# Kernel tuning notes

Measured on AMD Instinct MI355X. Metric: run time of the kernel, lower is better.

## Reference

```python
import jax, jax.numpy as jnp
import numpy as np

B, L, D, H, NL, FUT, MD = 4096, 64, 16, 128, 2, 30, 2
HEAD_IN = D + H  # 144


def setup_inputs() -> dict:
    key = jax.random.key(0)
    ks = jax.random.split(key, 20)
    g = lambda k, *sh: jax.random.normal(k, sh, dtype=jnp.float32) * 0.05
    return {
        'history': jax.random.normal(ks[0], (B, L, D), dtype=jnp.float32),
        'history_mask': jnp.ones((B, L), dtype=jnp.float32),
        'Wp': g(ks[1], D, H), 'bp': jnp.zeros((H,), jnp.float32),
        # stacked gate weights: order [f, i, o, c]
        'Wx': g(ks[2], NL, 4, H, H), 'bx': jnp.zeros((NL, 4, H), jnp.float32),
        'Uh': g(ks[3], NL, 4, H, H),
        'Wd': g(ks[4], NL, H, H), 'bd': jnp.zeros((NL, H), jnp.float32),
        'Wt': g(ks[5], NL, H), 'bt': jnp.zeros((NL, H), jnp.float32),
        'ln_g': jnp.ones((HEAD_IN,), jnp.float32), 'ln_b': jnp.zeros((HEAD_IN,), jnp.float32),
        'W1': g(ks[6], HEAD_IN, H), 'b1': jnp.zeros((H,), jnp.float32),
        'W2': g(ks[7], H, FUT * MD), 'b2': jnp.zeros((FUT * MD,), jnp.float32),
    }


def _forward(history, history_mask, Wp, bp, Wx, bx, Uh, Wd, bd, Wt, bt,
             ln_g, ln_b, W1, b1, W2, b2):
    x = history @ Wp + bp                                 # [B,L,H]
    delta = jnp.clip(history[..., 5], 0.0)[..., None]     # [B,L,1]
    mask = history_mask[..., None]                        # [B,L,1]
    e = jnp.float32(np.e)

    def step(carry, inp):
        h, c = carry                                      # each [NL,B,H]
        xt, dt, mt = inp                                  # [B,H],[B,1],[B,1]
        decay = 1.0 / jnp.log(e + dt)                     # [B,1]
        step_in = xt
        hs, cs = [], []
        for l in range(NL):
            z = (jnp.einsum('bh,ghk->gbk', step_in, Wx[l]) + bx[l][:, None, :]
                 + jnp.einsum('bh,ghk->gbk', h[l], Uh[l]))  # [4,B,H]
            f_t = jax.nn.sigmoid(z[0])
            i_t = jax.nn.sigmoid(z[1])
            o_t = jax.nn.sigmoid(z[2])
            c_tilde = jnp.tanh(z[3])
            h_tilde = c_tilde + i_t
            h_short = jnp.tanh(h_tilde @ Wd[l] + bd[l])
            d_t = jax.nn.sigmoid(decay * Wt[l] + bt[l])   # [B,H]
            h_star = (h_tilde - h_short) + h_short * d_t
            c_new = jnp.tanh(h_star + o_t * c[l])
            h_new = o_t * jnp.tanh(c_new)
            h_l = mt * h_new + (1.0 - mt) * h[l]
            c_l = mt * c_new + (1.0 - mt) * c[l]
            hs.append(h_l)
            cs.append(c_l)
            step_in = h_l
        return (jnp.stack(hs), jnp.stack(cs)), step_in

    h0 = jnp.zeros((NL, B, H), x.dtype)
    c0 = jnp.zeros((NL, B, H), x.dtype)
    xs = (x.transpose(1, 0, 2), delta.transpose(1, 0, 2), mask.transpose(1, 0, 2))
    _, outs = jax.lax.scan(step, (h0, c0), xs)            # [L,B,H]
    encoded = outs.transpose(1, 0, 2) * mask              # [B,L,H]

    # decoder state: last valid obs + hidden
    counts = jnp.clip(history_mask.sum(axis=1), 1, L).astype(jnp.int32)
    last = counts - 1
    bi = jnp.arange(B)
    state = jnp.concatenate([history[bi, last, :], encoded[bi, last, :]], axis=-1)

    # forecast head: LayerNorm -> Linear -> ReLU -> Linear
    mu = state.mean(axis=-1, keepdims=True)
    var = state.var(axis=-1, keepdims=True)
    sn = (state - mu) * jax.lax.rsqrt(var + 1e-5) * ln_g + ln_b
    pred = jax.nn.relu(sn @ W1 + b1) @ W2 + b2
    pred = pred.reshape(B, FUT, MD)
    return jnp.nan_to_num(pred, nan=0.0, posinf=1e4, neginf=-1e4)


def reference(history, history_mask, Wp, bp, Wx, bx, Uh, Wd, bd, Wt, bt,
              ln_g, ln_b, W1, b1, W2, b2):
    return _forward(history, history_mask, Wp, bp, Wx, bx, Uh, Wd, bd, Wt, bt,
                    ln_g, ln_b, W1, b1, W2, b2)
```

## Files before the change

### kernel.cpp

```cpp
#include <hip/hip_runtime.h>
#include <hip/hip_bf16.h>


typedef __bf16 bf16x8 __attribute__((ext_vector_type(8)));
typedef float  f32x4  __attribute__((ext_vector_type(4)));

__device__ __forceinline__ f32x4 mfma16(bf16x8 a, bf16x8 b, f32x4 c) {
  return __builtin_amdgcn_mfma_f32_16x16x32_bf16(a, b, c, 0, 0, 0);
}

#if __has_builtin(__builtin_amdgcn_exp2f)
__device__ __forceinline__ float fexp2(float x) { return __builtin_amdgcn_exp2f(x); }
#else
__device__ __forceinline__ float fexp2(float x) { return exp2f(x); }
#endif
#if __has_builtin(__builtin_amdgcn_rcpf)
__device__ __forceinline__ float frcp(float x) { return __builtin_amdgcn_rcpf(x); }
#else
__device__ __forceinline__ float frcp(float x) { return __fdividef(1.f, x); }
#endif
__device__ __forceinline__ float sigmE(float u) { return frcp(1.f + fexp2(u)); }
__device__ __forceinline__ float tanhE(float u) {
  return __fmaf_rn(-2.f, frcp(1.f + fexp2(u)), 1.f);
}
#define SCL_S (-1.44269504f)
#define SCL_T (2.88539008f)

#define OFF_BWD0 122880
#define OFF_BT1  155648
#define OFF_BWD1 352256
#define OFF_BZ0  385024

#define S_WB0   0
#define S_AH    122880
#define S_A0H   125440
#define S_A1H   129792
#define S_AT0   134144
#define S_AT1   138496
#define S_DM    142848
#define S_LAST  143232
#define S_TOTAL 143296
#define S_STATE 0
#define S_A1L   9216
#define S_REDS  17408
#define S_REDQ  18432

__device__ __forceinline__ int bt0f_off(int n, int k) {
  int g = n >> 7, w = (n >> 4) & 7, c = n & 15;
  int kk = k >> 5, q = (k >> 3) & 3, j = k & 7;
  return ((w * 3 + g) * 5 + kk) * 512 + (q * 16 + c) * 8 + j;
}

__global__ void tlstm_prep(const float* __restrict__ Wp, const float* __restrict__ bp,
                           const float* __restrict__ Wx, const float* __restrict__ bx,
                           const float* __restrict__ Uh, const float* __restrict__ Wd,
                           __bf16* __restrict__ BT0f, __bf16* __restrict__ BWd0,
                           __bf16* __restrict__ BT1, __bf16* __restrict__ BWd1,
                           float* __restrict__ bz0) {
  if (blockIdx.x < 26) {
    int idx = blockIdx.x * 256 + threadIdx.x;
    if (idx >= 384 * 17) return;
    int kk = idx / 384, n = idx - kk * 384;
    int npr = n & 127, g = n >> 7, gs = g + 1;
    float sg = (g == 2) ? SCL_T : SCL_S;
    const float* wxg = Wx + (gs * 128) * 128 + npr;
    if (kk < 16) {
      const float* wprow = Wp + kk * 128;
      float s = 0.f;
      for (int h = 0; h < 128; ++h) s += wprow[h] * wxg[h * 128];
      BT0f[bt0f_off(n, kk)] = (__bf16)(s * sg);
    } else {
      float s = bx[gs * 128 + npr];
      for (int h = 0; h < 128; ++h) s += bp[h] * wxg[h * 128];
      bz0[n] = s * sg;
      for (int k2 = 16; k2 < 32; ++k2) BT0f[bt0f_off(n, k2)] = (__bf16)0.f;
    }
    return;
  }
  int e = (blockIdx.x - 26) * 256 + threadIdx.x;
  if (e < 49152) {
    int k = e / 384, n = e - k * 384;
    int npr = n & 127, g = n >> 7, gs = g + 1;
    float sg = (g == 2) ? SCL_T : SCL_S;
    BT0f[bt0f_off(n, k + 32)] = (__bf16)(Uh[(gs * 128 + k) * 128 + npr] * sg);
  } else if (e < 65536) {
    int e2 = e - 49152; int k = e2 >> 7, n = e2 & 127;
    BWd0[n * 128 + k] = (__bf16)(Wd[k * 128 + n] * SCL_T);
  } else if (e < 163840) {
    int e2 = e - 65536; int k = e2 / 384, n = e2 - k * 384;
    int npr = n & 127, g = n >> 7, gs = g + 1;
    float sg = (g == 2) ? SCL_T : SCL_S;
    float v = (k < 128) ? Wx[((4 + gs) * 128 + k) * 128 + npr]
                        : Uh[((4 + gs) * 128 + (k - 128)) * 128 + npr];
    BT1[n * 256 + k] = (__bf16)(v * sg);
  } else if (e < 180224) {
    int e2 = e - 163840; int k = e2 >> 7, n = e2 & 127;
    BWd1[n * 128 + k] = (__bf16)(Wd[(128 + k) * 128 + n] * SCL_T);
  }
}

__global__ __launch_bounds__(512, 1) void tlstm_main(
    const float* __restrict__ hist, const float* __restrict__ hmask,
    const __bf16* __restrict__ BT0f, const __bf16* __restrict__ BWd0,
    const __bf16* __restrict__ BT1, const __bf16* __restrict__ BWd1,
    const float* __restrict__ bz0, const float* __restrict__ bx,
    const float* __restrict__ bd, const float* __restrict__ Wt,
    const float* __restrict__ bt, const float* __restrict__ lng,
    const float* __restrict__ lnb, const float* __restrict__ W1,
    const float* __restrict__ b1, const float* __restrict__ W2,
    const float* __restrict__ b2, float* __restrict__ out) {
  extern __shared__ __align__(16) char smem[];
  __bf16* WB0 = (__bf16*)(smem + S_WB0);
  __bf16 (*AH)[16][40]  = (__bf16(*)[16][40])(smem + S_AH);
  __bf16 (*A0H)[136]    = (__bf16(*)[136])(smem + S_A0H);
  __bf16 (*A1H)[136]    = (__bf16(*)[136])(smem + S_A1H);
  __bf16 (*AT0)[136]    = (__bf16(*)[136])(smem + S_AT0);
  __bf16 (*AT1)[136]    = (__bf16(*)[136])(smem + S_AT1);
  float (*dmL)[2][16]   = (float(*)[2][16])(smem + S_DM);
  int*   lastL          = (int*)(smem + S_LAST);
  float (*stateL)[144]  = (float(*)[144])(smem + S_STATE);
  float (*a1L)[128]     = (float(*)[128])(smem + S_A1L);
  float (*redS)[16]     = (float(*)[16])(smem + S_REDS);
  float (*redQ)[16]     = (float(*)[16])(smem + S_REDQ);

  const int tid  = threadIdx.x;
  const int wave = tid >> 6;
  const int lane = tid & 63;
  const int q    = lane >> 4;
  const int c16  = lane & 15;
  const int q8   = q * 8;
  const int b0   = blockIdx.x * 16;
  const int nc   = wave * 16 + c16;

  for (int i = tid * 8; i < 61440; i += 4096)
    *(bf16x8*)(WB0 + i) = *(const bf16x8*)(BT0f + i);
  {
    __bf16* z = (__bf16*)(smem + S_AH);
    for (int i = tid; i < 5632; i += 512) z[i] = (__bf16)0.f;
  }
  if (tid < 16) {
    float s = 0.f;
    for (int t = 0; t < 64; ++t) s += hmask[(b0 + tid) * 64 + t];
    s = fminf(fmaxf(s, 1.f), 64.f);
    lastL[tid] = (int)s - 1;
  }

  float bz0r[3], bz1r[3];
#pragma unroll
  for (int g = 0; g < 3; ++g) {
    float sg = (g == 2) ? SCL_T : SCL_S;
    bz0r[g] = bz0[g * 128 + nc];
    bz1r[g] = bx[(5 + g) * 128 + nc] * sg;
  }
  const float bd0r = bd[nc] * SCL_T,       bd1r = bd[128 + nc] * SCL_T;
  const float wt0r = Wt[nc] * SCL_S,       wt1r = Wt[128 + nc] * SCL_S;
  const float bt0r = bt[nc] * SCL_S,       bt1r = bt[128 + nc] * SCL_S;

  int offW[3];
#pragma unroll
  for (int g = 0; g < 3; ++g) offW[g] = ((wave * 3 + g) * 5) * 512 + lane * 8;

  bf16x8 wf1[24], bwd0[4], bwd1[4];
#pragma unroll
  for (int g = 0; g < 3; ++g)
#pragma unroll
    for (int kk = 0; kk < 8; ++kk)
      wf1[g * 8 + kk] = *(const bf16x8*)(BT1 + (g * 128 + nc) * 256 + kk * 32 + q8);
#pragma unroll
  for (int kk = 0; kk < 4; ++kk) {
    bwd0[kk] = *(const bf16x8*)(BWd0 + nc * 128 + q8 + kk * 32);
    bwd1[kk] = *(const bf16x8*)(BWd1 + nc * 128 + q8 + kk * 32);
  }

  float h0r[4] = {}, c0r[4] = {}, h1r[4] = {}, c1r[4] = {}, encr[4] = {};

  __syncthreads();

  int lrow[4];
#pragma unroll
  for (int r = 0; r < 4; ++r) lrow[r] = lastL[q * 4 + r];

  const int srow = (tid >> 4) & 15, scol = tid & 15;
  const float* histrow = hist + (long)(b0 + srow) * 1024 + scol;
  const float* hmrow   = hmask + (long)(b0 + srow) * 64;

  float hv = 0.f, mv = 0.f;
  if (tid < 256) {
    float v0 = histrow[0];
    AH[0][srow][scol] = (__bf16)v0;
    if (scol == 5)
      dmL[0][0][srow] = __fdividef(1.f, __logf(2.7182818284590452f + fmaxf(v0, 0.f)));
    if (scol == 0) dmL[0][1][srow] = hmrow[0];
    hv = histrow[16];
    mv = hmrow[1];
  }
  __syncthreads();

  for (int t = 0; t <= 64; ++t) {
    const int p = t & 1, pn = p ^ 1;
    const int sp = t % 3, sm = (t + 2) % 3, sn = (t + 1) % 3;

    float otl0[4], otl1[4];
    if (t > 0) {
      f32x4 acc[3];
#pragma unroll
      for (int g = 0; g < 3; ++g) acc[g] = (f32x4){bz1r[g], bz1r[g], bz1r[g], bz1r[g]};
#pragma unroll
      for (int kk = 0; kk < 4; ++kk) {
        bf16x8 a = *(const bf16x8*)&A0H[c16][kk * 32 + q8];
#pragma unroll
        for (int g = 0; g < 3; ++g) acc[g] = mfma16(a, wf1[g * 8 + kk], acc[g]);
      }
#pragma unroll
      for (int kk = 0; kk < 4; ++kk) {
        bf16x8 a = *(const bf16x8*)&A1H[c16][kk * 32 + q8];
#pragma unroll
        for (int g = 0; g < 3; ++g) acc[g] = mfma16(a, wf1[g * 8 + 4 + kk], acc[g]);
      }
#pragma unroll
      for (int r = 0; r < 4; ++r) {
        float ht = tanhE(acc[2][r]) + sigmE(acc[0][r]);
        otl1[r] = sigmE(acc[1][r]);
        AT1[q * 4 + r][nc] = (__bf16)ht;
      }
    }
    if (t < 64) {
      f32x4 acc[3];
#pragma unroll
      for (int g = 0; g < 3; ++g) acc[g] = (f32x4){bz0r[g], bz0r[g], bz0r[g], bz0r[g]};
      {
        bf16x8 a = *(const bf16x8*)&AH[p][c16][q8];
#pragma unroll
        for (int g = 0; g < 3; ++g)
          acc[g] = mfma16(a, *(const bf16x8*)(WB0 + offW[g]), acc[g]);
      }
#pragma unroll
      for (int kk = 0; kk < 4; ++kk) {
        bf16x8 a = *(const bf16x8*)&A0H[c16][kk * 32 + q8];
#pragma unroll
        for (int g = 0; g < 3; ++g)
          acc[g] = mfma16(a, *(const bf16x8*)(WB0 + offW[g] + (kk + 1) * 512), acc[g]);
      }
#pragma unroll
      for (int r = 0; r < 4; ++r) {
        float ht = tanhE(acc[2][r]) + sigmE(acc[0][r]);
        otl0[r] = sigmE(acc[1][r]);
        AT0[q * 4 + r][nc] = (__bf16)ht;
      }
    }
    __syncthreads();

    if (t < 64) {
      float drow[4], mrow[4];
#pragma unroll
      for (int r = 0; r < 4; ++r) {
        drow[r] = dmL[sp][0][q * 4 + r];
        mrow[r] = dmL[sp][1][q * 4 + r];
      }
      f32x4 accd = (f32x4){bd0r, bd0r, bd0r, bd0r};
#pragma unroll
      for (int kk = 0; kk < 4; ++kk) {
        bf16x8 a = *(const bf16x8*)&AT0[c16][kk * 32 + q8];
        accd = mfma16(a, bwd0[kk], accd);
      }
#pragma unroll
      for (int r = 0; r < 4; ++r) {
        float htl   = (float)AT0[q * 4 + r][nc];
        float hs    = tanhE(accd[r]);
        float dgate = sigmE(__fmaf_rn(drow[r], wt0r, bt0r));
        float hstar = __fmaf_rn(hs, dgate - 1.f, htl);
        float cn    = tanhE(SCL_T * __fmaf_rn(otl0[r], c0r[r], hstar));
        float hn    = otl0[r] * tanhE(SCL_T * cn);
        float m     = mrow[r];
        float hl    = __fmaf_rn(m, hn - h0r[r], h0r[r]);
        float cl    = __fmaf_rn(m, cn - c0r[r], c0r[r]);
        h0r[r] = hl; c0r[r] = cl;
        A0H[q * 4 + r][nc] = (__bf16)hl;
      }
    }
    if (t > 0) {
      float dpre[4], mpre[4];
#pragma unroll
      for (int r = 0; r < 4; ++r) {
        dpre[r] = dmL[sm][0][q * 4 + r];
        mpre[r] = dmL[sm][1][q * 4 + r];
      }
      f32x4 accd = (f32x4){bd1r, bd1r, bd1r, bd1r};
#pragma unroll
      for (int kk = 0; kk < 4; ++kk) {
        bf16x8 a = *(const bf16x8*)&AT1[c16][kk * 32 + q8];
        accd = mfma16(a, bwd1[kk], accd);
      }
      const int tm1 = t - 1;
#pragma unroll
      for (int r = 0; r < 4; ++r) {
        float htl   = (float)AT1[q * 4 + r][nc];
        float hs    = tanhE(accd[r]);
        float dgate = sigmE(__fmaf_rn(dpre[r], wt1r, bt1r));
        float hstar = __fmaf_rn(hs, dgate - 1.f, htl);
        float cn    = tanhE(SCL_T * __fmaf_rn(otl1[r], c1r[r], hstar));
        float hn    = otl1[r] * tanhE(SCL_T * cn);
        float m     = mpre[r];
        float hl    = __fmaf_rn(m, hn - h1r[r], h1r[r]);
        float cl    = __fmaf_rn(m, cn - c1r[r], c1r[r]);
        h1r[r] = hl; c1r[r] = cl;
        A1H[q * 4 + r][nc] = (__bf16)hl;
        if (tm1 == lrow[r]) encr[r] = hl * m;
      }
    }
    if (tid < 256 && t < 63) {
      AH[pn][srow][scol] = (__bf16)hv;
      if (scol == 5)
        dmL[sn][0][srow] = __fdividef(1.f, __logf(2.7182818284590452f + fmaxf(hv, 0.f)));
      if (scol == 0) dmL[sn][1][srow] = mv;
      if (t < 62) { hv = histrow[(t + 2) * 16]; mv = hmrow[t + 2]; }
    }
    __syncthreads();
  }

  if (tid < 256)
    stateL[srow][scol] = hist[((long)(b0 + srow) * 64 + lastL[srow]) * 16 + scol];
#pragma unroll
  for (int r = 0; r < 4; ++r)
    stateL[q * 4 + r][16 + nc] = encr[r];
  __syncthreads();

  if (tid < 256) {
    float sm2 = 0.f, sq = 0.f;
    for (int k = scol; k < 144; k += 16) {
      float v = stateL[srow][k];
      sm2 += v; sq += v * v;
    }
    redS[srow][scol] = sm2; redQ[srow][scol] = sq;
  }
  __syncthreads();
  if (tid < 16) {
    float sm2 = 0.f, sq = 0.f;
    for (int s2 = 0; s2 < 16; ++s2) { sm2 += redS[tid][s2]; sq += redQ[tid][s2]; }
    float mu  = sm2 * (1.f / 144.f);
    float var = sq * (1.f / 144.f) - mu * mu;
    redS[0][tid] = mu;
    redQ[0][tid] = rsqrtf(var + 1e-5f);
  }
  __syncthreads();
  if (tid < 256) {
    float mu = redS[0][srow], rs = redQ[0][srow];
    for (int k = scol; k < 144; k += 16)
      stateL[srow][k] = (stateL[srow][k] - mu) * rs * lng[k] + lnb[k];
  }
  __syncthreads();
  if (tid < 256) {
    float accw[8];
#pragma unroll
    for (int o = 0; o < 8; ++o) accw[o] = b1[scol + 16 * o];
    for (int k = 0; k < 144; ++k) {
      float sv = stateL[srow][k];
      const float* w = W1 + k * 128 + scol;
#pragma unroll
      for (int o = 0; o < 8; ++o) accw[o] += sv * w[16 * o];
    }
#pragma unroll
    for (int o = 0; o < 8; ++o) a1L[srow][scol + 16 * o] = fmaxf(accw[o], 0.f);
  }
  __syncthreads();
  for (int e = tid; e < 960; e += 512) {
    int row = e / 60, j = e - row * 60;
    float accv = b2[j];
    for (int k = 0; k < 128; ++k) accv += a1L[row][k] * W2[k * 60 + j];
    accv = (accv != accv) ? 0.f : fminf(fmaxf(accv, -1e4f), 1e4f);
    out[(b0 + row) * 60 + j] = accv;
  }
}

extern "C" void kernel_launch(void* const* d_in, const int* in_sizes, int n_in,
                              void* d_out, int out_size, void* d_ws, size_t ws_size,
                              hipStream_t stream) {
  const float* hist  = (const float*)d_in[0];
  const float* hmask = (const float*)d_in[1];
  const float* Wp    = (const float*)d_in[2];
  const float* bp    = (const float*)d_in[3];
  const float* Wx    = (const float*)d_in[4];
  const float* bx    = (const float*)d_in[5];
  const float* Uh    = (const float*)d_in[6];
  const float* Wd    = (const float*)d_in[7];
  const float* bd    = (const float*)d_in[8];
  const float* Wt    = (const float*)d_in[9];
  const float* bt    = (const float*)d_in[10];
  const float* lng   = (const float*)d_in[11];
  const float* lnb   = (const float*)d_in[12];
  const float* W1    = (const float*)d_in[13];
  const float* b1    = (const float*)d_in[14];
  const float* W2    = (const float*)d_in[15];
  const float* b2    = (const float*)d_in[16];
  float* out = (float*)d_out;

  char* ws = (char*)d_ws;
  __bf16* BT0f = (__bf16*)ws;
  __bf16* BWd0 = (__bf16*)(ws + OFF_BWD0);
  __bf16* BT1  = (__bf16*)(ws + OFF_BT1);
  __bf16* BWd1 = (__bf16*)(ws + OFF_BWD1);
  float*  bz0  = (float*)(ws + OFF_BZ0);

  hipFuncSetAttribute((const void*)tlstm_main,
                      hipFuncAttributeMaxDynamicSharedMemorySize, S_TOTAL);

  tlstm_prep<<<730, 256, 0, stream>>>(Wp, bp, Wx, bx, Uh, Wd,
                                      BT0f, BWd0, BT1, BWd1, bz0);
  tlstm_main<<<256, 512, S_TOTAL, stream>>>(hist, hmask, BT0f, BWd0, BT1, BWd1,
                                            bz0, bx, bd, Wt, bt, lng, lnb,
                                            W1, b1, W2, b2, out);
}
```

Baseline: 300.1 us.

## Split the two LSTM layers across separate wave groups in a 1024-thread block

Doubles the block to 1024 threads and gives layer 0 to waves 0-7 and layer 1 to waves 8-15, so each wave runs one layer's MFMA and elementwise work per step instead of both. Each thread now keeps only one layer's weights and state in registers, which relieves register pressure, and the two layers' work runs on different waves inside the same barrier-delimited phases. The cost is twice as many waves to synchronise at each barrier and a register budget capped by the 1024-thread launch bound, which may cause spills in the layer-1 group that holds 24 weight fragments.

```diff
diff --git a/kernel.cpp b/kernel.cpp
--- a/kernel.cpp
+++ b/kernel.cpp
@@ -99,7 +99,7 @@
   }
 }
 
-__global__ __launch_bounds__(512, 1) void tlstm_main(
+__global__ __launch_bounds__(1024, 1) void tlstm_main(
     const float* __restrict__ hist, const float* __restrict__ hmask,
     const __bf16* __restrict__ BT0f, const __bf16* __restrict__ BWd0,
     const __bf16* __restrict__ BT1, const __bf16* __restrict__ BWd1,
@@ -124,19 +124,20 @@
   float (*redQ)[16]     = (float(*)[16])(smem + S_REDQ);
 
   const int tid  = threadIdx.x;
-  const int wave = tid >> 6;
+  const int grp  = tid >> 9;
+  const int w8   = (tid >> 6) & 7;
   const int lane = tid & 63;
   const int q    = lane >> 4;
   const int c16  = lane & 15;
   const int q8   = q * 8;
   const int b0   = blockIdx.x * 16;
-  const int nc   = wave * 16 + c16;
-
-  for (int i = tid * 8; i < 61440; i += 4096)
+  const int nc   = w8 * 16 + c16;
+
+  for (int i = tid * 8; i < 61440; i += 8192)
     *(bf16x8*)(WB0 + i) = *(const bf16x8*)(BT0f + i);
   {
     __bf16* z = (__bf16*)(smem + S_AH);
-    for (int i = tid; i < 5632; i += 512) z[i] = (__bf16)0.f;
+    for (int i = tid; i < 5632; i += 1024) z[i] = (__bf16)0.f;
   }
   if (tid < 16) {
     float s = 0.f;
@@ -145,34 +146,42 @@
     lastL[tid] = (int)s - 1;
   }
 
-  float bz0r[3], bz1r[3];
-#pragma unroll
-  for (int g = 0; g < 3; ++g) {
-    float sg = (g == 2) ? SCL_T : SCL_S;
-    bz0r[g] = bz0[g * 128 + nc];
-    bz1r[g] = bx[(5 + g) * 128 + nc] * sg;
-  }
-  const float bd0r = bd[nc] * SCL_T,       bd1r = bd[128 + nc] * SCL_T;
-  const float wt0r = Wt[nc] * SCL_S,       wt1r = Wt[128 + nc] * SCL_S;
-  const float bt0r = bt[nc] * SCL_S,       bt1r = bt[128 + nc] * SCL_S;
+  const int lo = grp * 128;
+  float bzr[3];
+  if (grp == 0) {
+#pragma unroll
+    for (int g = 0; g < 3; ++g) bzr[g] = bz0[g * 128 + nc];
+  } else {
+#pragma unroll
+    for (int g = 0; g < 3; ++g) {
+      float sg = (g == 2) ? SCL_T : SCL_S;
+      bzr[g] = bx[(5 + g) * 128 + nc] * sg;
+    }
+  }
+  const float bdr = bd[lo + nc] * SCL_T;
+  const float wtr = Wt[lo + nc] * SCL_S;
+  const float btr = bt[lo + nc] * SCL_S;
 
   int offW[3];
-#pragma unroll
-  for (int g = 0; g < 3; ++g) offW[g] = ((wave * 3 + g) * 5) * 512 + lane * 8;
-
-  bf16x8 wf1[24], bwd0[4], bwd1[4];
-#pragma unroll
-  for (int g = 0; g < 3; ++g)
-#pragma unroll
-    for (int kk = 0; kk < 8; ++kk)
-      wf1[g * 8 + kk] = *(const bf16x8*)(BT1 + (g * 128 + nc) * 256 + kk * 32 + q8);
-#pragma unroll
-  for (int kk = 0; kk < 4; ++kk) {
-    bwd0[kk] = *(const bf16x8*)(BWd0 + nc * 128 + q8 + kk * 32);
-    bwd1[kk] = *(const bf16x8*)(BWd1 + nc * 128 + q8 + kk * 32);
-  }
-
-  float h0r[4] = {}, c0r[4] = {}, h1r[4] = {}, c1r[4] = {}, encr[4] = {};
+  bf16x8 wf1[24], bwd[4];
+  if (grp == 0) {
+#pragma unroll
+    for (int g = 0; g < 3; ++g) offW[g] = ((w8 * 3 + g) * 5) * 512 + lane * 8;
+#pragma unroll
+    for (int kk = 0; kk < 4; ++kk)
+      bwd[kk] = *(const bf16x8*)(BWd0 + nc * 128 + q8 + kk * 32);
+  } else {
+#pragma unroll
+    for (int g = 0; g < 3; ++g)
+#pragma unroll
+      for (int kk = 0; kk < 8; ++kk)
+        wf1[g * 8 + kk] = *(const bf16x8*)(BT1 + (g * 128 + nc) * 256 + kk * 32 + q8);
+#pragma unroll
+    for (int kk = 0; kk < 4; ++kk)
+      bwd[kk] = *(const bf16x8*)(BWd1 + nc * 128 + q8 + kk * 32);
+  }
+
+  float hr[4] = {}, cr[4] = {}, encr[4] = {};
 
   __syncthreads();
 
@@ -200,129 +209,137 @@
     const int p = t & 1, pn = p ^ 1;
     const int sp = t % 3, sm = (t + 2) % 3, sn = (t + 1) % 3;
 
-    float otl0[4], otl1[4];
-    if (t > 0) {
-      f32x4 acc[3];
-#pragma unroll
-      for (int g = 0; g < 3; ++g) acc[g] = (f32x4){bz1r[g], bz1r[g], bz1r[g], bz1r[g]};
-#pragma unroll
-      for (int kk = 0; kk < 4; ++kk) {
-        bf16x8 a = *(const bf16x8*)&A0H[c16][kk * 32 + q8];
-#pragma unroll
-        for (int g = 0; g < 3; ++g) acc[g] = mfma16(a, wf1[g * 8 + kk], acc[g]);
+    float otl[4];
+    if (grp == 0) {
+      if (t < 64) {
+        f32x4 acc[3];
+#pragma unroll
+        for (int g = 0; g < 3; ++g) acc[g] = (f32x4){bzr[g], bzr[g], bzr[g], bzr[g]};
+        {
+          bf16x8 a = *(const bf16x8*)&AH[p][c16][q8];
+#pragma unroll
+          for (int g = 0; g < 3; ++g)
+            acc[g] = mfma16(a, *(const bf16x8*)(WB0 + offW[g]), acc[g]);
+        }
+#pragma unroll
+        for (int kk = 0; kk < 4; ++kk) {
+          bf16x8 a = *(const bf16x8*)&A0H[c16][kk * 32 + q8];
+#pragma unroll
+          for (int g = 0; g < 3; ++g)
+            acc[g] = mfma16(a, *(const bf16x8*)(WB0 + offW[g] + (kk + 1) * 512), acc[g]);
+        }
+#pragma unroll
+        for (int r = 0; r < 4; ++r) {
+          float ht = tanhE(acc[2][r]) + sigmE(acc[0][r]);
+          otl[r] = sigmE(acc[1][r]);
+          AT0[q * 4 + r][nc] = (__bf16)ht;
+        }
       }
-#pragma unroll
-      for (int kk = 0; kk < 4; ++kk) {
-        bf16x8 a = *(const bf16x8*)&A1H[c16][kk * 32 + q8];
-#pragma unroll
-        for (int g = 0; g < 3; ++g) acc[g] = mfma16(a, wf1[g * 8 + 4 + kk], acc[g]);
+    } else {
+      if (t > 0) {
+        f32x4 acc[3];
+#pragma unroll
+        for (int g = 0; g < 3; ++g) acc[g] = (f32x4){bzr[g], bzr[g], bzr[g], bzr[g]};
+#pragma unroll
+        for (int kk = 0; kk < 4; ++kk) {
+          bf16x8 a = *(const bf16x8*)&A0H[c16][kk * 32 + q8];
+#pragma unroll
+          for (int g = 0; g < 3; ++g) acc[g] = mfma16(a, wf1[g * 8 + kk], acc[g]);
+        }
+#pragma unroll
+        for (int kk = 0; kk < 4; ++kk) {
+          bf16x8 a = *(const bf16x8*)&A1H[c16][kk * 32 + q8];
+#pragma unroll
+          for (int g = 0; g < 3; ++g) acc[g] = mfma16(a, wf1[g * 8 + 4 + kk], acc[g]);
+        }
+#pragma unroll
+        for (int r = 0; r < 4; ++r) {
+          float ht = tanhE(acc[2][r]) + sigmE(acc[0][r]);
+          otl[r] = sigmE(acc[1][r]);
+          AT1[q * 4 + r][nc] = (__bf16)ht;
+        }
       }
-#pragma unroll
-      for (int r = 0; r < 4; ++r) {
-        float ht = tanhE(acc[2][r]) + sigmE(acc[0][r]);
-        otl1[r] = sigmE(acc[1][r]);
-        AT1[q * 4 + r][nc] = (__bf16)ht;
+    }
+    __syncthreads();
+
+    if (grp == 0) {
+      if (t < 64) {
+        float drow[4], mrow[4];
+#pragma unroll
+        for (int r = 0; r < 4; ++r) {
+          drow[r] = dmL[sp][0][q * 4 + r];
+          mrow[r] = dmL[sp][1][q * 4 + r];
+        }
+        f32x4 accd = (f32x4){bdr, bdr, bdr, bdr};
+#pragma unroll
+        for (int kk = 0; kk < 4; ++kk) {
+          bf16x8 a = *(const bf16x8*)&AT0[c16][kk * 32 + q8];
+          accd = mfma16(a, bwd[kk], accd);
+        }
+#pragma unroll
+        for (int r = 0; r < 4; ++r) {
+          float htl   = (float)AT0[q * 4 + r][nc];
+          float hs    = tanhE(accd[r]);
+          float dgate = sigmE(__fmaf_rn(drow[r], wtr, btr));
+          float hstar = __fmaf_rn(hs, dgate - 1.f, htl);
+          float cn    = tanhE(SCL_T * __fmaf_rn(otl[r], cr[r], hstar));
+          float hn    = otl[r] * tanhE(SCL_T * cn);
+          float m     = mrow[r];
+          float hl    = __fmaf_rn(m, hn - hr[r], hr[r]);
+          float cl    = __fmaf_rn(m, cn - cr[r], cr[r]);
+          hr[r] = hl; cr[r] = cl;
+          A0H[q * 4 + r][nc] = (__bf16)hl;
+        }
       }
-    }
-    if (t < 64) {
-      f32x4 acc[3];
-#pragma unroll
-      for (int g = 0; g < 3; ++g) acc[g] = (f32x4){bz0r[g], bz0r[g], bz0r[g], bz0r[g]};
-      {
-        bf16x8 a = *(const bf16x8*)&AH[p][c16][q8];
-#pragma unroll
-        for (int g = 0; g < 3; ++g)
-          acc[g] = mfma16(a, *(const bf16x8*)(WB0 + offW[g]), acc[g]);
+      if (tid < 256 && t < 63) {
+        AH[pn][srow][scol] = (__bf16)hv;
+        if (scol == 5)
+          dmL[sn][0][srow] = __fdividef(1.f, __logf(2.7182818284590452f + fmaxf(hv, 0.f)));
+        if (scol == 0) dmL[sn][1][srow] = mv;
+        if (t < 62) { hv = histrow[(t + 2) * 16]; mv = hmrow[t + 2]; }
       }
-#pragma unroll
-      for (int kk = 0; kk < 4; ++kk) {
-        bf16x8 a = *(const bf16x8*)&A0H[c16][kk * 32 + q8];
-#pragma unroll
-        for (int g = 0; g < 3; ++g)
-          acc[g] = mfma16(a, *(const bf16x8*)(WB0 + offW[g] + (kk + 1) * 512), acc[g]);
+    } else {
+      if (t > 0) {
+        float dpre[4], mpre[4];
+#pragma unroll
+        for (int r = 0; r < 4; ++r) {
+          dpre[r] = dmL[sm][0][q * 4 + r];
+          mpre[r] = dmL[sm][1][q * 4 + r];
+        }
+        f32x4 accd = (f32x4){bdr, bdr, bdr, bdr};
+#pragma unroll
+        for (int kk = 0; kk < 4; ++kk) {
+          bf16x8 a = *(const bf16x8*)&AT1[c16][kk * 32 + q8];
+          accd = mfma16(a, bwd[kk], accd);
+        }
+        const int tm1 = t - 1;
+#pragma unroll
+        for (int r = 0; r < 4; ++r) {
+          float htl   = (float)AT1[q * 4 + r][nc];
+          float hs    = tanhE(accd[r]);
+          float dgate = sigmE(__fmaf_rn(dpre[r], wtr, btr));
+          float hstar = __fmaf_rn(hs, dgate - 1.f, htl);
+          float cn    = tanhE(SCL_T * __fmaf_rn(otl[r], cr[r], hstar));
+          float hn    = otl[r] * tanhE(SCL_T * cn);
+          float m     = mpre[r];
+          float hl    = __fmaf_rn(m, hn - hr[r], hr[r]);
+          float cl    = __fmaf_rn(m, cn - cr[r], cr[r]);
+          hr[r] = hl; cr[r] = cl;
+          A1H[q * 4 + r][nc] = (__bf16)hl;
+          if (tm1 == lrow[r]) encr[r] = hl * m;
+        }
       }
-#pragma unroll
-      for (int r = 0; r < 4; ++r) {
-        float ht = tanhE(acc[2][r]) + sigmE(acc[0][r]);
-        otl0[r] = sigmE(acc[1][r]);
-        AT0[q * 4 + r][nc] = (__bf16)ht;
-      }
-    }
-    __syncthreads();
-
-    if (t < 64) {
-      float drow[4], mrow[4];
-#pragma unroll
-      for (int r = 0; r < 4; ++r) {
-        drow[r] = dmL[sp][0][q * 4 + r];
-        mrow[r] = dmL[sp][1][q * 4 + r];
-      }
-      f32x4 accd = (f32x4){bd0r, bd0r, bd0r, bd0r};
-#pragma unroll
-      for (int kk = 0; kk < 4; ++kk) {
-        bf16x8 a = *(const bf16x8*)&AT0[c16][kk * 32 + q8];
-        accd = mfma16(a, bwd0[kk], accd);
-      }
-#pragma unroll
-      for (int r = 0; r < 4; ++r) {
-        float htl   = (float)AT0[q * 4 + r][nc];
-        float hs    = tanhE(accd[r]);
-        float dgate = sigmE(__fmaf_rn(drow[r], wt0r, bt0r));
-        float hstar = __fmaf_rn(hs, dgate - 1.f, htl);
-        float cn    = tanhE(SCL_T * __fmaf_rn(otl0[r], c0r[r], hstar));
-        float hn    = otl0[r] * tanhE(SCL_T * cn);
-        float m     = mrow[r];
-        float hl    = __fmaf_rn(m, hn - h0r[r], h0r[r]);
-        float cl    = __fmaf_rn(m, cn - c0r[r], c0r[r]);
-        h0r[r] = hl; c0r[r] = cl;
-        A0H[q * 4 + r][nc] = (__bf16)hl;
-      }
-    }
-    if (t > 0) {
-      float dpre[4], mpre[4];
-#pragma unroll
-      for (int r = 0; r < 4; ++r) {
-        dpre[r] = dmL[sm][0][q * 4 + r];
-        mpre[r] = dmL[sm][1][q * 4 + r];
-      }
-      f32x4 accd = (f32x4){bd1r, bd1r, bd1r, bd1r};
-#pragma unroll
-      for (int kk = 0; kk < 4; ++kk) {
-        bf16x8 a = *(const bf16x8*)&AT1[c16][kk * 32 + q8];
-        accd = mfma16(a, bwd1[kk], accd);
-      }
-      const int tm1 = t - 1;
-#pragma unroll
-      for (int r = 0; r < 4; ++r) {
-        float htl   = (float)AT1[q * 4 + r][nc];
-        float hs    = tanhE(accd[r]);
-        float dgate = sigmE(__fmaf_rn(dpre[r], wt1r, bt1r));
-        float hstar = __fmaf_rn(hs, dgate - 1.f, htl);
-        float cn    = tanhE(SCL_T * __fmaf_rn(otl1[r], c1r[r], hstar));
-        float hn    = otl1[r] * tanhE(SCL_T * cn);
-        float m     = mpre[r];
-        float hl    = __fmaf_rn(m, hn - h1r[r], h1r[r]);
-        float cl    = __fmaf_rn(m, cn - c1r[r], c1r[r]);
-        h1r[r] = hl; c1r[r] = cl;
-        A1H[q * 4 + r][nc] = (__bf16)hl;
-        if (tm1 == lrow[r]) encr[r] = hl * m;
-      }
-    }
-    if (tid < 256 && t < 63) {
-      AH[pn][srow][scol] = (__bf16)hv;
-      if (scol == 5)
-        dmL[sn][0][srow] = __fdividef(1.f, __logf(2.7182818284590452f + fmaxf(hv, 0.f)));
-      if (scol == 0) dmL[sn][1][srow] = mv;
-      if (t < 62) { hv = histrow[(t + 2) * 16]; mv = hmrow[t + 2]; }
     }
     __syncthreads();
   }
 
   if (tid < 256)
     stateL[srow][scol] = hist[((long)(b0 + srow) * 64 + lastL[srow]) * 16 + scol];
-#pragma unroll
-  for (int r = 0; r < 4; ++r)
-    stateL[q * 4 + r][16 + nc] = encr[r];
+  if (grp == 1) {
+#pragma unroll
+    for (int r = 0; r < 4; ++r)
+      stateL[q * 4 + r][16 + nc] = encr[r];
+  }
   __syncthreads();
 
   if (tid < 256) {
@@ -363,7 +380,7 @@
     for (int o = 0; o < 8; ++o) a1L[srow][scol + 16 * o] = fmaxf(accw[o], 0.f);
   }
   __syncthreads();
-  for (int e = tid; e < 960; e += 512) {
+  for (int e = tid; e < 960; e += 1024) {
     int row = e / 60, j = e - row * 60;
     float accv = b2[j];
     for (int k = 0; k < 128; ++k) accv += a1L[row][k] * W2[k * 60 + j];
@@ -406,7 +423,7 @@
 
   tlstm_prep<<<730, 256, 0, stream>>>(Wp, bp, Wx, bx, Uh, Wd,
                                       BT0f, BWd0, BT1, BWd1, bz0);
-  tlstm_main<<<256, 512, S_TOTAL, stream>>>(hist, hmask, BT0f, BWd0, BT1, BWd1,
-                                            bz0, bx, bd, Wt, bt, lng, lnb,
-                                            W1, b1, W2, b2, out);
-}
+  tlstm_main<<<256, 1024, S_TOTAL, stream>>>(hist, hmask, BT0f, BWd0, BT1, BWd1,
+                                             bz0, bx, bd, Wt, bt, lng, lnb,
+                                             W1, b1, W2, b2, out);
+}
```

Result: slower. 584.8 us (+94.8%).
